# Kernel tuning notes

Hardware: AMD Instinct MI355X
Metric: run time of the kernel (lower is better)

The kernel has to match this reference:

```python
import jax, jax.numpy as jnp
import numpy as np

B, S, D = 4, 2048, 256
H = 8
KD = D  # keras MHA key_dim = input_shape[-1] -> per-head dim equals D
EPS = 1e-5


def layer_norm(x, gamma, beta):
    mu = jnp.mean(x, axis=-1, keepdims=True)
    var = jnp.var(x, axis=-1, keepdims=True)
    return (x - mu) * jax.lax.rsqrt(var + EPS) * gamma + beta


def setup_inputs() -> dict:
    key = jax.random.key(0)
    ks = jax.random.split(key, 12)
    scale = 1.0 / np.sqrt(D)
    inp = {
        "input_query": jax.random.normal(ks[0], (B, S, D), jnp.float32),
        "key": jax.random.normal(ks[1], (B, S, D), jnp.float32),
        "value": jax.random.normal(ks[2], (B, S, D), jnp.float32),
        # LayerNorm params (3 separate norms)
        "gq": jnp.ones((D,), jnp.float32), "bq_ln": jnp.zeros((D,), jnp.float32),
        "gk": jnp.ones((D,), jnp.float32), "bk_ln": jnp.zeros((D,), jnp.float32),
        "gv": jnp.ones((D,), jnp.float32), "bv_ln": jnp.zeros((D,), jnp.float32),
        # MHA projection weights: [D, H, KD] for q/k/v, [H, KD, D] for output
        "Wq": jax.random.normal(ks[3], (D, H, KD), jnp.float32) * scale,
        "bq": jnp.zeros((H, KD), jnp.float32),
        "Wk": jax.random.normal(ks[4], (D, H, KD), jnp.float32) * scale,
        "bk": jnp.zeros((H, KD), jnp.float32),
        "Wv": jax.random.normal(ks[5], (D, H, KD), jnp.float32) * scale,
        "bv": jnp.zeros((H, KD), jnp.float32),
        "Wo": jax.random.normal(ks[6], (H, KD, D), jnp.float32) * scale,
        "bo": jnp.zeros((D,), jnp.float32),
    }
    return inp


def reference(input_query, key, value, gq, bq_ln, gk, bk_ln, gv, bv_ln,
              Wq, bq, Wk, bk, Wv, bv, Wo, bo):
    # pre-LN on each stream
    q_in = layer_norm(input_query, gq, bq_ln)
    k_in = layer_norm(key, gk, bk_ln)
    v_in = layer_norm(value, gv, bv_ln)

    # projections -> [B, S, H, KD]
    q = jnp.einsum('bsd,dhk->bshk', q_in, Wq) + bq
    k = jnp.einsum('bsd,dhk->bshk', k_in, Wk) + bk
    v = jnp.einsum('bsd,dhk->bshk', v_in, Wv) + bv

    # scaled dot-product attention (keras scales query by 1/sqrt(key_dim))
    q = q * (1.0 / np.sqrt(KD)).astype(np.float32)
    scores = jnp.einsum('bqhk,bshk->bhqs', q, k)  # [B, H, Sq, Sk]
    probs = jax.nn.softmax(scores, axis=-1)
    # dropout = 0.0 (inference)
    attn = jnp.einsum('bhqs,bshk->bqhk', probs, v)
    out = jnp.einsum('bqhk,hkd->bqd', attn, Wo) + bo

    return input_query + out
```

## Files before the change

kernel.cpp:

```cpp
#include <hip/hip_runtime.h>

using bf16x8 = __attribute__((ext_vector_type(8))) __bf16;
using f32x4  = __attribute__((ext_vector_type(4))) float;
using f32x16 = __attribute__((ext_vector_type(16))) float;
using uint2v = __attribute__((ext_vector_type(2))) unsigned;
typedef unsigned short u16;
typedef const __attribute__((address_space(1))) void* gas_p;
typedef __attribute__((address_space(3))) void* las_p;

#define LOG2E 1.4426950408889634f

__device__ __forceinline__ u16 f2bf(float f) {
  union { float f; unsigned u; } v; v.f = f;
  unsigned r = v.u + 0x7fffu + ((v.u >> 16) & 1u);
  return (u16)(r >> 16);
}

__device__ __forceinline__ unsigned pkbf(float a, float b) {
  unsigned r;
  asm("v_cvt_pk_bf16_f32 %0, %1, %2" : "=v"(r) : "v"(a), "v"(b));
  return r;
}

__device__ __forceinline__ float exp2v(float x) {
  float r;
  asm("v_exp_f32 %0, %1" : "=v"(r) : "v"(x));
  return r;
}

__device__ __forceinline__ unsigned pk_fp8x4(float a, float b, float c, float d) {
  int w = __builtin_amdgcn_cvt_pk_fp8_f32(a, b, 0, false);
  w = __builtin_amdgcn_cvt_pk_fp8_f32(c, d, w, true);
  return (unsigned)w;
}

__device__ __forceinline__ uint2v swap32(unsigned a, unsigned b) {
  return __builtin_amdgcn_permlane32_swap(a, b, false, false);
}

__device__ __forceinline__ void gload16(const void* g, void* l) {
  __builtin_amdgcn_global_load_lds((gas_p)g, (las_p)l, 16, 0, 0);
}

#define MFMA(a, b, c)   __builtin_amdgcn_mfma_f32_16x16x32_bf16((a), (b), (c), 0, 0, 0)
#define MFMA32(a, b, c) __builtin_amdgcn_mfma_f32_32x32x16_bf16((a), (b), (c), 0, 0, 0)
#define MFMA8(a, b, c)  __builtin_amdgcn_mfma_f32_32x32x16_fp8_fp8((a), (b), (c), 0, 0, 0)

__global__ __launch_bounds__(256) void transpose_conv(
    const float* __restrict__ Wq, const float* __restrict__ Wk,
    const float* __restrict__ Wv, const float* __restrict__ Wo,
    u16* __restrict__ wqt, u16* __restrict__ wkt,
    u16* __restrict__ wvt, u16* __restrict__ wot)
{
  int z = blockIdx.y;
  const float* src = (z == 0) ? Wq : (z == 1) ? Wk : (z == 2) ? Wv : Wo;
  u16* dst = (z == 0) ? wqt : (z == 1) ? wkt : (z == 2) ? wvt : wot;
  int C = (z < 3) ? 2048 : 256;
  int R = (z < 3) ? 256 : 2048;
  int TC = C >> 5;
  int tc = blockIdx.x % TC, tr = blockIdx.x / TC;
  __shared__ float tile[32][33];
  int j = threadIdx.x & 31, i0 = threadIdx.x >> 5;
#pragma unroll
  for (int p = 0; p < 4; p++)
    tile[i0 + p * 8][j] = src[(tr * 32 + i0 + p * 8) * C + tc * 32 + j];
  __syncthreads();
#pragma unroll
  for (int p = 0; p < 4; p++)
    dst[(tc * 32 + i0 + p * 8) * R + tr * 32 + j] = f2bf(tile[j][i0 + p * 8]);
}

__global__ __launch_bounds__(256) void ln3_kernel(
    const float* __restrict__ xq, const float* __restrict__ xk, const float* __restrict__ xv,
    const float* __restrict__ gq, const float* __restrict__ bq,
    const float* __restrict__ gk, const float* __restrict__ bk,
    const float* __restrict__ gv, const float* __restrict__ bv,
    u16* __restrict__ oq, u16* __restrict__ ok, u16* __restrict__ ov)
{
  int z = blockIdx.y;
  const float* x = (z == 0) ? xq : (z == 1) ? xk : xv;
  const float* g = (z == 0) ? gq : (z == 1) ? gk : gv;
  const float* be = (z == 0) ? bq : (z == 1) ? bk : bv;
  u16* o = (z == 0) ? oq : (z == 1) ? ok : ov;
  int w = threadIdx.x >> 6, l = threadIdx.x & 63;
  int row = blockIdx.x * 4 + w;
  float4 x4 = *(const float4*)(x + row * 256 + l * 4);
  float s = x4.x + x4.y + x4.z + x4.w;
  float sq = x4.x * x4.x + x4.y * x4.y + x4.z * x4.z + x4.w * x4.w;
#pragma unroll
  for (int mm = 1; mm < 64; mm <<= 1) { s += __shfl_xor(s, mm); sq += __shfl_xor(sq, mm); }
  float mu = s * (1.f / 256.f);
  float var = sq * (1.f / 256.f) - mu * mu;
  float rs = rsqrtf(var + 1e-5f);
  float4 g4 = *(const float4*)(g + l * 4);
  float4 b4 = *(const float4*)(be + l * 4);
  ushort4 o4;
  o4.x = f2bf((x4.x - mu) * rs * g4.x + b4.x);
  o4.y = f2bf((x4.y - mu) * rs * g4.y + b4.y);
  o4.z = f2bf((x4.z - mu) * rs * g4.z + b4.z);
  o4.w = f2bf((x4.w - mu) * rs * g4.w + b4.w);
  *(ushort4*)(o + row * 256 + l * 4) = o4;
}

__global__ __launch_bounds__(256) void proj_gemm_qk(
    const u16* __restrict__ qn, const u16* __restrict__ kn,
    const u16* __restrict__ wqt, const u16* __restrict__ wkt,
    const float* __restrict__ bq, const float* __restrict__ bk,
    u16* __restrict__ qo, u16* __restrict__ ko)
{
  __shared__ u16 As[128 * 64];
  __shared__ u16 Bs[128 * 64];
  int z = blockIdx.z;
  const u16* A  = z ? kn : qn;
  const u16* Bt = z ? wkt : wqt;
  const float* bias = z ? bk : bq;
  u16* Co = z ? ko : qo;
  float scale = z ? 1.0f : 0.0625f * LOG2E;

  int i0 = blockIdx.x * 128, n0 = blockIdx.y * 128;
  int tid = threadIdx.x, w = tid >> 6, l = tid & 63;
  int wr = w >> 1, wc = w & 1, l15 = l & 15, qv = l >> 4;

  f32x4 acc[4][4] = {};

  for (int k0 = 0; k0 < 256; k0 += 64) {
    __syncthreads();
#pragma unroll
    for (int j = 0; j < 4; j++) {
      int c = (w * 4 + j) * 64 + l;
      int row = c >> 3, co = (c & 7) * 8;
      gload16(A + (i0 + row) * 256 + k0 + co, (char*)As + (w * 4 + j) * 1024);
      gload16(Bt + (n0 + row) * 256 + k0 + co, (char*)Bs + (w * 4 + j) * 1024);
    }
    __syncthreads();
#pragma unroll
    for (int kk = 0; kk < 2; kk++) {
      bf16x8 a[4], bfr[4];
#pragma unroll
      for (int m = 0; m < 4; m++)
        a[m] = *(const bf16x8*)(As + (wr * 64 + m * 16 + l15) * 64 + kk * 32 + qv * 8);
#pragma unroll
      for (int n = 0; n < 4; n++)
        bfr[n] = *(const bf16x8*)(Bs + (wc * 64 + n * 16 + l15) * 64 + kk * 32 + qv * 8);
#pragma unroll
      for (int m = 0; m < 4; m++)
#pragma unroll
        for (int n = 0; n < 4; n++) acc[m][n] = MFMA(bfr[n], a[m], acc[m][n]);
    }
  }

#pragma unroll
  for (int m = 0; m < 4; m++) {
    int row = i0 + wr * 64 + m * 16 + l15;
    int bb = row >> 11, ss = row & 2047;
#pragma unroll
    for (int n = 0; n < 4; n++) {
      int col0 = n0 + wc * 64 + n * 16 + qv * 4;
      float4 bc4 = *(const float4*)(bias + col0);
      int hd = col0 >> 8, kd0 = col0 & 255;
      ushort4 o4;
      o4.x = f2bf((acc[m][n][0] + bc4.x) * scale);
      o4.y = f2bf((acc[m][n][1] + bc4.y) * scale);
      o4.z = f2bf((acc[m][n][2] + bc4.z) * scale);
      o4.w = f2bf((acc[m][n][3] + bc4.w) * scale);
      *(ushort4*)(Co + ((size_t)(bb * 8 + hd) * 2048 + ss) * 256 + kd0) = o4;
    }
  }
}

__global__ __launch_bounds__(256) void proj_gemm_v(
    const u16* __restrict__ vn, const u16* __restrict__ wvt,
    const float* __restrict__ bv, unsigned char* __restrict__ vo)
{
  __shared__ u16 As[128 * 64];
  __shared__ u16 Bs[128 * 64];
  int i0 = blockIdx.x * 128, n0 = blockIdx.y * 128;
  int tid = threadIdx.x, w = tid >> 6, l = tid & 63;
  int wr = w >> 1, wc = w & 1, l15 = l & 15, qv = l >> 4;

  f32x4 acc[4][4] = {};

  for (int k0 = 0; k0 < 256; k0 += 64) {
    __syncthreads();
#pragma unroll
    for (int j = 0; j < 4; j++) {
      int c = (w * 4 + j) * 64 + l;
      int row = c >> 3, co = (c & 7) * 8;
      gload16(vn + (i0 + row) * 256 + k0 + co, (char*)As + (w * 4 + j) * 1024);
      gload16(wvt + (n0 + row) * 256 + k0 + co, (char*)Bs + (w * 4 + j) * 1024);
    }
    __syncthreads();
#pragma unroll
    for (int kk = 0; kk < 2; kk++) {
      bf16x8 a[4], bfr[4];
#pragma unroll
      for (int m = 0; m < 4; m++)
        a[m] = *(const bf16x8*)(As + (wr * 64 + m * 16 + l15) * 64 + kk * 32 + qv * 8);
#pragma unroll
      for (int n = 0; n < 4; n++)
        bfr[n] = *(const bf16x8*)(Bs + (wc * 64 + n * 16 + l15) * 64 + kk * 32 + qv * 8);
#pragma unroll
      for (int m = 0; m < 4; m++)
#pragma unroll
        for (int n = 0; n < 4; n++) acc[m][n] = MFMA(a[m], bfr[n], acc[m][n]);
    }
  }

#pragma unroll
  for (int n = 0; n < 4; n++) {
    int col = n0 + wc * 64 + n * 16 + l15;
    float bc = bv[col];
    int hd = col >> 8, kd = col & 255;
#pragma unroll
    for (int m = 0; m < 4; m++) {
      int row0 = i0 + wr * 64 + m * 16 + qv * 4;
      int bb = row0 >> 11, ss = row0 & 2047;
      unsigned wv = pk_fp8x4(acc[m][n][0] + bc, acc[m][n][1] + bc,
                             acc[m][n][2] + bc, acc[m][n][3] + bc);
      int pos = (ss & ~63) | (((ss >> 3) & 3) << 4) | (((ss >> 5) & 1) << 3) | (ss & 7);
      *(unsigned*)(vo + ((size_t)(bb * 8 + hd) * 256 + kd) * 2048 + pos) = wv;
    }
  }
}

__global__ __launch_bounds__(512, 2) void flash_attn(
    const u16* __restrict__ q, const u16* __restrict__ k,
    const unsigned char* __restrict__ vt, u16* __restrict__ o)
{
  __shared__ char lds[98304];
  int f = blockIdx.x;
  int qt = f >> 5;
  int bh = (f & 7) | (((f >> 3) & 3) << 3);
  int b = bh >> 3, hh = bh & 7;
  int tid = threadIdx.x, w = tid >> 6, l = tid & 63;
  int l31 = l & 31, h = l >> 5;

  const u16* Q = q + (size_t)(bh * 2048 + qt * 256 + w * 32) * 256;
  const u16* K = k + (size_t)bh * 2048 * 256;
  const unsigned char* V = vt + (size_t)bh * 256 * 2048;

  bf16x8 qf[16];
#pragma unroll
  for (int dt = 0; dt < 16; dt++)
    qf[dt] = *(const bf16x8*)(Q + l31 * 256 + dt * 16 + h * 8);

  f32x16 oacc[8] = {};
  float m_ = -1e30f, lsum = 0.f;

  auto stage = [&](int t, char* base) {
#pragma unroll
    for (int j = 0; j < 4; j++) {
      int c = w * 4 + j;
      int off = c * 1024 + l * 16;
      int r = off >> 9, ps = l & 31;
      gload16(K + (size_t)(t * 64 + r) * 256 + ((ps ^ (r & 31)) << 3), base + off);
    }
#pragma unroll
    for (int j = 0; j < 2; j++) {
      int c = w * 2 + j;
      int off = c * 1024 + l * 16;
      int r = off >> 8, pg = (off >> 4) & 15;
      int g = pg ^ (r & 15);
      int d = r + 64 * (g >> 2), sc = g & 3;
      gload16(V + (size_t)d * 2048 + t * 64 + sc * 16, base + 32768 + off);
    }
  };

  stage(0, lds);
  __syncthreads();

  for (int t = 0; t < 32; t++) {
    char* cur = lds + (size_t)(t & 1) * 49152;
    char* nxt = lds + (size_t)((t + 1) & 1) * 49152;
    if (t + 1 < 32) stage(t + 1, nxt);

    f32x16 p0 = {}, p1 = {};
    __builtin_amdgcn_s_setprio(1);
#pragma unroll
    for (int dt = 0; dt < 16; dt++) {
      int sl = ((dt * 2 + h) ^ l31) << 4;
      bf16x8 kf0 = *(const bf16x8*)(cur + l31 * 512 + sl);
      bf16x8 kf1 = *(const bf16x8*)(cur + (32 + l31) * 512 + sl);
      p0 = MFMA32(kf0, qf[dt], p0);
      p1 = MFMA32(kf1, qf[dt], p1);
    }
    __builtin_amdgcn_s_setprio(0);

    float n0 = fmaxf(fmaxf(p0[0], p0[1]), fmaxf(p0[2], p0[3]));
    float n1 = fmaxf(fmaxf(p0[4], p0[5]), fmaxf(p0[6], p0[7]));
    float n2 = fmaxf(fmaxf(p0[8], p0[9]), fmaxf(p0[10], p0[11]));
    float n3 = fmaxf(fmaxf(p0[12], p0[13]), fmaxf(p0[14], p0[15]));
    float n4 = fmaxf(fmaxf(p1[0], p1[1]), fmaxf(p1[2], p1[3]));
    float n5 = fmaxf(fmaxf(p1[4], p1[5]), fmaxf(p1[6], p1[7]));
    float n6 = fmaxf(fmaxf(p1[8], p1[9]), fmaxf(p1[10], p1[11]));
    float n7 = fmaxf(fmaxf(p1[12], p1[13]), fmaxf(p1[14], p1[15]));
    float mt = fmaxf(fmaxf(fmaxf(n0, n1), fmaxf(n2, n3)),
                     fmaxf(fmaxf(n4, n5), fmaxf(n6, n7)));
    {
      uint2v mr = swap32(__builtin_bit_cast(unsigned, mt), __builtin_bit_cast(unsigned, mt));
      mt = fmaxf(__builtin_bit_cast(float, mr.x), __builtin_bit_cast(float, mr.y));
    }
    if (__any(mt > m_ + 7.0f)) {
      float mn = fmaxf(m_, mt);
      float fsc = exp2v(m_ - mn);
      lsum *= fsc;
#pragma unroll
      for (int dt = 0; dt < 8; dt++)
#pragma unroll
        for (int i = 0; i < 16; i++) oacc[dt][i] *= fsc;
      m_ = mn;
    }
#pragma unroll
    for (int i = 0; i < 16; i++) { p0[i] = exp2v(p0[i] - m_); lsum += p0[i]; }
#pragma unroll
    for (int i = 0; i < 16; i++) { p1[i] = exp2v(p1[i] - m_); lsum += p1[i]; }

    unsigned pwf0[4], pwf1[4];
#pragma unroll
    for (int j = 0; j < 4; j++) {
      pwf0[j] = pk_fp8x4(p0[4 * j], p0[4 * j + 1], p0[4 * j + 2], p0[4 * j + 3]);
      pwf1[j] = pk_fp8x4(p1[4 * j], p1[4 * j + 1], p1[4 * j + 2], p1[4 * j + 3]);
    }

#pragma unroll
    for (int k2 = 0; k2 < 2; k2++) {
      uint2v f0 = swap32(pwf0[k2 * 2], pwf0[k2 * 2 + 1]);
      uint2v f1 = swap32(pwf1[k2 * 2], pwf1[k2 * 2 + 1]);
      long long pA = (long long)(((unsigned long long)f0.y << 32) | f0.x);
      long long pB = (long long)(((unsigned long long)f1.y << 32) | f1.x);
      __builtin_amdgcn_s_setprio(1);
#pragma unroll
      for (int dt = 0; dt < 8; dt++) {
        int r = (dt & 1) * 32 + l31;
        int g = (dt >> 1) * 4 + k2 * 2 + h;
        const uint4 vv = *(const uint4*)(cur + 32768 + r * 256 + ((g ^ (r & 15)) << 4));
        long long vA = (long long)(((unsigned long long)vv.y << 32) | vv.x);
        long long vB = (long long)(((unsigned long long)vv.w << 32) | vv.z);
        oacc[dt] = MFMA8(vA, pA, oacc[dt]);
        oacc[dt] = MFMA8(vB, pB, oacc[dt]);
      }
      __builtin_amdgcn_s_setprio(0);
    }

    asm volatile("s_waitcnt vmcnt(0)" ::: "memory");
    __syncthreads();
  }

  __syncthreads();
  float lsc;
  {
    uint2v lr = swap32(__builtin_bit_cast(unsigned, lsum), __builtin_bit_cast(unsigned, lsum));
    lsc = __builtin_bit_cast(float, lr.x) + __builtin_bit_cast(float, lr.y);
  }
  float inv = 1.0f / lsc;
  char* wbase = (char*)lds + w * 8192;
  int qr15 = l31 & 15;
#pragma unroll
  for (int ph = 0; ph < 2; ph++) {
    if ((l31 >> 4) == ph) {
#pragma unroll
      for (int dt = 0; dt < 8; dt++) {
#pragma unroll
        for (int rg = 0; rg < 4; rg++) {
          uint2 uu;
          uu.x = pkbf(oacc[dt][rg * 4 + 0] * inv, oacc[dt][rg * 4 + 1] * inv);
          uu.y = pkbf(oacc[dt][rg * 4 + 2] * inv, oacc[dt][rg * 4 + 3] * inv);
          *(uint2*)(wbase + qr15 * 512 + ((dt * 64 + rg * 16) ^ (qr15 << 4)) + h * 8) = uu;
        }
      }
    }
    asm volatile("s_waitcnt lgkmcnt(0)" ::: "memory");
    __builtin_amdgcn_sched_barrier(0);
#pragma unroll
    for (int c = 0; c < 8; c++) {
      int qr = c * 2 + h;
      uint4 vv = *(const uint4*)(wbase + qr * 512 + ((l31 ^ qr) << 4));
      int s = qt * 256 + w * 32 + ph * 16 + qr;
      *(uint4*)((char*)o + (size_t)(b * 2048 + s) * 4096 + hh * 512 + l31 * 16) = vv;
    }
    asm volatile("s_waitcnt lgkmcnt(0)" ::: "memory");
  }
}

__global__ __launch_bounds__(256) void out_gemm(
    const u16* __restrict__ A, const u16* __restrict__ Bt,
    const float* __restrict__ bo, const float* __restrict__ resid,
    float* __restrict__ out)
{
  __shared__ u16 As[128 * 64];
  __shared__ u16 Bs[64 * 64];
  int i0 = blockIdx.x * 128, n0 = blockIdx.y * 64;
  int tid = threadIdx.x, w = tid >> 6, l = tid & 63, l15 = l & 15, qv = l >> 4;

  f32x4 acc[2][4] = {};

  for (int k0 = 0; k0 < 2048; k0 += 64) {
    __syncthreads();
#pragma unroll
    for (int j = 0; j < 4; j++) {
      int c = (w * 4 + j) * 64 + l;
      int row = c >> 3, co = (c & 7) * 8;
      gload16(A + (i0 + row) * 2048 + k0 + co, (char*)As + (w * 4 + j) * 1024);
    }
#pragma unroll
    for (int j = 0; j < 2; j++) {
      int c = (w * 2 + j) * 64 + l;
      int row = c >> 3, co = (c & 7) * 8;
      gload16(Bt + (n0 + row) * 2048 + k0 + co, (char*)Bs + (w * 2 + j) * 1024);
    }
    __syncthreads();
#pragma unroll
    for (int kk = 0; kk < 2; kk++) {
      bf16x8 a[2], bfr[4];
#pragma unroll
      for (int m = 0; m < 2; m++)
        a[m] = *(const bf16x8*)(As + (w * 32 + m * 16 + l15) * 64 + kk * 32 + qv * 8);
#pragma unroll
      for (int n = 0; n < 4; n++)
        bfr[n] = *(const bf16x8*)(Bs + (n * 16 + l15) * 64 + kk * 32 + qv * 8);
#pragma unroll
      for (int m = 0; m < 2; m++)
#pragma unroll
        for (int n = 0; n < 4; n++) acc[m][n] = MFMA(bfr[n], a[m], acc[m][n]);
    }
  }

#pragma unroll
  for (int m = 0; m < 2; m++) {
    int row = i0 + w * 32 + m * 16 + l15;
#pragma unroll
    for (int n = 0; n < 4; n++) {
      int col0 = n0 + n * 16 + qv * 4;
      float4 bc4 = *(const float4*)(bo + col0);
      float4 rs4 = *(const float4*)(resid + (size_t)row * 256 + col0);
      float4 o4;
      o4.x = acc[m][n][0] + bc4.x + rs4.x;
      o4.y = acc[m][n][1] + bc4.y + rs4.y;
      o4.z = acc[m][n][2] + bc4.z + rs4.z;
      o4.w = acc[m][n][3] + bc4.w + rs4.w;
      *(float4*)(out + (size_t)row * 256 + col0) = o4;
    }
  }
}

extern "C" void kernel_launch(void* const* d_in, const int* in_sizes, int n_in,
                              void* d_out, int out_size, void* d_ws, size_t ws_size,
                              hipStream_t stream)
{
  const float* inq  = (const float*)d_in[0];
  const float* key  = (const float*)d_in[1];
  const float* val  = (const float*)d_in[2];
  const float* gq   = (const float*)d_in[3];
  const float* bqln = (const float*)d_in[4];
  const float* gk   = (const float*)d_in[5];
  const float* bkln = (const float*)d_in[6];
  const float* gv   = (const float*)d_in[7];
  const float* bvln = (const float*)d_in[8];
  const float* Wq   = (const float*)d_in[9];
  const float* bq   = (const float*)d_in[10];
  const float* Wk   = (const float*)d_in[11];
  const float* bk   = (const float*)d_in[12];
  const float* Wv   = (const float*)d_in[13];
  const float* bv   = (const float*)d_in[14];
  const float* Wo   = (const float*)d_in[15];
  const float* bo   = (const float*)d_in[16];

  char* ws = (char*)d_ws;
  const size_t MB = 1ull << 20;
  u16* wqt = (u16*)(ws + 0 * MB);
  u16* wkt = (u16*)(ws + 1 * MB);
  u16* wvt = (u16*)(ws + 2 * MB);
  u16* wot = (u16*)(ws + 3 * MB);
  u16* qn  = (u16*)(ws + 4 * MB);
  u16* kn  = (u16*)(ws + 8 * MB);
  u16* vn  = (u16*)(ws + 12 * MB);
  u16* qws = (u16*)(ws + 16 * MB);
  u16* kws = (u16*)(ws + 48 * MB);
  u16* attn = (u16*)(ws + 80 * MB);
  unsigned char* vtw = (unsigned char*)(ws + 112 * MB);

  transpose_conv<<<dim3(512, 4), 256, 0, stream>>>(Wq, Wk, Wv, Wo, wqt, wkt, wvt, wot);
  ln3_kernel<<<dim3(2048, 3), 256, 0, stream>>>(inq, key, val, gq, bqln, gk, bkln, gv, bvln,
                                                qn, kn, vn);
  proj_gemm_qk<<<dim3(64, 16, 2), 256, 0, stream>>>(qn, kn, wqt, wkt, bq, bk, qws, kws);
  proj_gemm_v<<<dim3(64, 16), 256, 0, stream>>>(vn, wvt, bv, vtw);
  flash_attn<<<256, 512, 0, stream>>>(qws, kws, vtw, attn);
  out_gemm<<<dim3(64, 4), 256, 0, stream>>>(attn, wot, bo, inq, (float*)d_out);
}
```

Baseline: 255.4 us.

## Split flash-attention tile into two 32-key halves with staggered wave order

Splits each 64-key tile into two 32-key halves, each running its own QK^T, online softmax and PV, and changes the V fp8 position permutation so each half maps to a contiguous P fragment. Waves 4-7 process the halves in the opposite order to waves 0-3, so MFMA and softmax phases interleave across waves and LDS bank use is spread out. Two independent accumulators in QK^T shorten the MFMA dependency chain. The cost is a max-reduction and rescale check per half instead of per tile, which adds extra rescale work.

Measured after the change: 273.0 us. +6.9%, slower.

```diff
diff --git a/kernel.cpp b/kernel.cpp
--- a/kernel.cpp
+++ b/kernel.cpp
@@ -217,7 +217,8 @@
       int bb = row0 >> 11, ss = row0 & 2047;
       unsigned wv = pk_fp8x4(acc[m][n][0] + bc, acc[m][n][1] + bc,
                              acc[m][n][2] + bc, acc[m][n][3] + bc);
-      int pos = (ss & ~63) | (((ss >> 3) & 3) << 4) | (((ss >> 5) & 1) << 3) | (ss & 7);
+      int pos = (ss & ~63) | (((ss >> 5) & 1) << 5) | (((ss >> 3) & 1) << 4)
+              | (((ss >> 4) & 1) << 3) | (ss & 7);
       *(unsigned*)(vo + ((size_t)(bb * 8 + hd) * 256 + kd) * 2048 + pos) = wv;
     }
   }
@@ -234,6 +235,7 @@
   int b = bh >> 3, hh = bh & 7;
   int tid = threadIdx.x, w = tid >> 6, l = tid & 63;
   int l31 = l & 31, h = l >> 5;
+  int ho = (w >> 2) & 1;
 
   const u16* Q = q + (size_t)(bh * 2048 + qt * 256 + w * 32) * 256;
   const u16* K = k + (size_t)bh * 2048 * 256;
@@ -274,65 +276,63 @@
     char* nxt = lds + (size_t)((t + 1) & 1) * 49152;
     if (t + 1 < 32) stage(t + 1, nxt);
 
-    f32x16 p0 = {}, p1 = {};
-    __builtin_amdgcn_s_setprio(1);
-#pragma unroll
-    for (int dt = 0; dt < 16; dt++) {
-      int sl = ((dt * 2 + h) ^ l31) << 4;
-      bf16x8 kf0 = *(const bf16x8*)(cur + l31 * 512 + sl);
-      bf16x8 kf1 = *(const bf16x8*)(cur + (32 + l31) * 512 + sl);
-      p0 = MFMA32(kf0, qf[dt], p0);
-      p1 = MFMA32(kf1, qf[dt], p1);
-    }
-    __builtin_amdgcn_s_setprio(0);
-
-    float n0 = fmaxf(fmaxf(p0[0], p0[1]), fmaxf(p0[2], p0[3]));
-    float n1 = fmaxf(fmaxf(p0[4], p0[5]), fmaxf(p0[6], p0[7]));
-    float n2 = fmaxf(fmaxf(p0[8], p0[9]), fmaxf(p0[10], p0[11]));
-    float n3 = fmaxf(fmaxf(p0[12], p0[13]), fmaxf(p0[14], p0[15]));
-    float n4 = fmaxf(fmaxf(p1[0], p1[1]), fmaxf(p1[2], p1[3]));
-    float n5 = fmaxf(fmaxf(p1[4], p1[5]), fmaxf(p1[6], p1[7]));
-    float n6 = fmaxf(fmaxf(p1[8], p1[9]), fmaxf(p1[10], p1[11]));
-    float n7 = fmaxf(fmaxf(p1[12], p1[13]), fmaxf(p1[14], p1[15]));
-    float mt = fmaxf(fmaxf(fmaxf(n0, n1), fmaxf(n2, n3)),
-                     fmaxf(fmaxf(n4, n5), fmaxf(n6, n7)));
-    {
-      uint2v mr = swap32(__builtin_bit_cast(unsigned, mt), __builtin_bit_cast(unsigned, mt));
-      mt = fmaxf(__builtin_bit_cast(float, mr.x), __builtin_bit_cast(float, mr.y));
-    }
-    if (__any(mt > m_ + 7.0f)) {
-      float mn = fmaxf(m_, mt);
-      float fsc = exp2v(m_ - mn);
-      lsum *= fsc;
-#pragma unroll
-      for (int dt = 0; dt < 8; dt++)
-#pragma unroll
-        for (int i = 0; i < 16; i++) oacc[dt][i] *= fsc;
-      m_ = mn;
-    }
-#pragma unroll
-    for (int i = 0; i < 16; i++) { p0[i] = exp2v(p0[i] - m_); lsum += p0[i]; }
-#pragma unroll
-    for (int i = 0; i < 16; i++) { p1[i] = exp2v(p1[i] - m_); lsum += p1[i]; }
-
-    unsigned pwf0[4], pwf1[4];
-#pragma unroll
-    for (int j = 0; j < 4; j++) {
-      pwf0[j] = pk_fp8x4(p0[4 * j], p0[4 * j + 1], p0[4 * j + 2], p0[4 * j + 3]);
-      pwf1[j] = pk_fp8x4(p1[4 * j], p1[4 * j + 1], p1[4 * j + 2], p1[4 * j + 3]);
-    }
-
-#pragma unroll
-    for (int k2 = 0; k2 < 2; k2++) {
-      uint2v f0 = swap32(pwf0[k2 * 2], pwf0[k2 * 2 + 1]);
-      uint2v f1 = swap32(pwf1[k2 * 2], pwf1[k2 * 2 + 1]);
+    auto half = [&](int hf) {
+      int row = hf * 32 + l31;
+      f32x16 pa = {}, pb = {};
+      __builtin_amdgcn_s_setprio(1);
+#pragma unroll
+      for (int dd = 0; dd < 8; dd++) {
+        bf16x8 kfE = *(const bf16x8*)(cur + row * 512 + ((((2 * dd) * 2 + h) ^ l31) << 4));
+        bf16x8 kfO = *(const bf16x8*)(cur + row * 512 + ((((2 * dd + 1) * 2 + h) ^ l31) << 4));
+        pa = MFMA32(kfE, qf[2 * dd], pa);
+        pb = MFMA32(kfO, qf[2 * dd + 1], pb);
+      }
+      __builtin_amdgcn_s_setprio(0);
+      f32x16 p = pa + pb;
+
+      float n0 = fmaxf(fmaxf(p[0], p[1]), fmaxf(p[2], p[3]));
+      float n1 = fmaxf(fmaxf(p[4], p[5]), fmaxf(p[6], p[7]));
+      float n2 = fmaxf(fmaxf(p[8], p[9]), fmaxf(p[10], p[11]));
+      float n3 = fmaxf(fmaxf(p[12], p[13]), fmaxf(p[14], p[15]));
+      float mt = fmaxf(fmaxf(n0, n1), fmaxf(n2, n3));
+      {
+        uint2v mr = swap32(__builtin_bit_cast(unsigned, mt), __builtin_bit_cast(unsigned, mt));
+        mt = fmaxf(__builtin_bit_cast(float, mr.x), __builtin_bit_cast(float, mr.y));
+      }
+      if (__any(mt > m_ + 7.0f)) {
+        float mn = fmaxf(m_, mt);
+        float fsc = exp2v(m_ - mn);
+        lsum *= fsc;
+#pragma unroll
+        for (int dt = 0; dt < 8; dt++)
+#pragma unroll
+          for (int i = 0; i < 16; i++) oacc[dt][i] *= fsc;
+        m_ = mn;
+      }
+      float s0 = 0.f, s1 = 0.f, s2 = 0.f, s3 = 0.f;
+#pragma unroll
+      for (int i = 0; i < 16; i += 4) {
+        p[i] = exp2v(p[i] - m_);         s0 += p[i];
+        p[i + 1] = exp2v(p[i + 1] - m_); s1 += p[i + 1];
+        p[i + 2] = exp2v(p[i + 2] - m_); s2 += p[i + 2];
+        p[i + 3] = exp2v(p[i + 3] - m_); s3 += p[i + 3];
+      }
+      lsum += (s0 + s1) + (s2 + s3);
+
+      unsigned pwf[4];
+#pragma unroll
+      for (int j = 0; j < 4; j++)
+        pwf[j] = pk_fp8x4(p[4 * j], p[4 * j + 1], p[4 * j + 2], p[4 * j + 3]);
+
+      uint2v f0 = swap32(pwf[0], pwf[1]);
+      uint2v f1 = swap32(pwf[2], pwf[3]);
       long long pA = (long long)(((unsigned long long)f0.y << 32) | f0.x);
       long long pB = (long long)(((unsigned long long)f1.y << 32) | f1.x);
       __builtin_amdgcn_s_setprio(1);
 #pragma unroll
       for (int dt = 0; dt < 8; dt++) {
         int r = (dt & 1) * 32 + l31;
-        int g = (dt >> 1) * 4 + k2 * 2 + h;
+        int g = (dt >> 1) * 4 + hf * 2 + h;
         const uint4 vv = *(const uint4*)(cur + 32768 + r * 256 + ((g ^ (r & 15)) << 4));
         long long vA = (long long)(((unsigned long long)vv.y << 32) | vv.x);
         long long vB = (long long)(((unsigned long long)vv.w << 32) | vv.z);
@@ -340,7 +340,10 @@
         oacc[dt] = MFMA8(vB, pB, oacc[dt]);
       }
       __builtin_amdgcn_s_setprio(0);
-    }
+    };
+
+    half(ho);
+    half(1 - ho);
 
     asm volatile("s_waitcnt vmcnt(0)" ::: "memory");
     __syncthreads();
```
